# Kernel tuning notes

Measured on AMD Instinct MI355X. Metric: run time of the kernel, lower is better.

Reference implementation:

```python
import jax, jax.numpy as jnp
import numpy as np

# Module config (matches init_kwargs)
B, C, T, H, W = 8, 64, 50, 64, 64
KH = KW = 2          # kernel_size
SH = SW = 2          # stride
DH = DW = 1          # dilation
HO = (H - (KH - 1) * DH - 1) // SH + 1  # 32
WO = (W - (KW - 1) * DW - 1) // SW + 1  # 32


def setup_inputs() -> dict:
    key = jax.random.key(0)
    x = jax.random.uniform(key, (B, C, T, H, W), dtype=jnp.float32)
    return {"x": x}


def reference(x):
    b, c, t, h, w = x.shape
    # temporal cumsum then sum over time (mode '2D')
    x_sum = jnp.cumsum(x, axis=2).sum(axis=2)  # (B, C, H, W)

    # max_pool2d with flat (row-major, per-channel H*W) indices, torch semantics
    hh = (jnp.arange(HO) * SH)[:, None] + jnp.arange(KH) * DH  # (HO, KH)
    ww = (jnp.arange(WO) * SW)[:, None] + jnp.arange(KW) * DW  # (WO, KW)
    win = x_sum[:, :, hh, :][..., ww]                     # (B, C, HO, KH, WO, KW)
    win = win.transpose(0, 1, 2, 4, 3, 5).reshape(b, c, HO, WO, KH * KW)
    # flat H*W index of each window element, row-major within window
    flat = (hh[:, None, :, None] * w + ww[None, :, None, :]).reshape(HO, WO, KH * KW)
    amax = jnp.argmax(win, axis=-1)                       # first max, like torch
    flat_b = jnp.broadcast_to(flat, (b, c, HO, WO, KH * KW))
    indices_2d = jnp.take_along_axis(flat_b, amax[..., None], axis=-1)[..., 0]  # (B,C,HO,WO)

    # gather the winning spatial location at every timestep
    x_flat = x.reshape(b, c, t, h * w)
    idx = jnp.broadcast_to(indices_2d.reshape(b, c, 1, HO * WO), (b, c, t, HO * WO))
    spk_rec = jnp.take_along_axis(x_flat, idx, axis=3).reshape(b, c, t, HO, WO)

    loss = 0.0 * spk_rec.mean()
    return spk_rec, loss
```

## Files before the change

kernel.cpp:

```cpp
#include <hip/hip_runtime.h>

#define BB 8
#define CC 64
#define TT 50
#define HH 64
#define WW 64
#define HO 32
#define WO 32
#define PLANE (HH * WW)
#define BC_STRIDE (TT * PLANE)
#define OUT_T_STRIDE (HO * WO)
#define OUT_BC_STRIDE (TT * OUT_T_STRIDE)
#define N_OUT_MAIN (BB * CC * OUT_BC_STRIDE)

__global__ __launch_bounds__(256, 3)
void spike_pool_kernel(const float* __restrict__ x, float* __restrict__ out) {
    const int blk = blockIdx.x;
    const int bc  = blk >> 3;
    const int R   = blk & 7;
    const int tid = threadIdx.x;

    const float2* __restrict__ base =
        (const float2*)(x + (size_t)bc * BC_STRIDE + R * 8 * WW);

    float2 pix[TT];
    float c0 = 0.f, c1 = 0.f, s0 = 0.f, s1 = 0.f;
#pragma unroll
    for (int t = 0; t < TT; ++t) {
        float2 v = base[(size_t)t * (PLANE / 2) + tid];
        pix[t] = v;
        c0 += v.x; s0 += c0;
        c1 += v.y; s1 += c1;
    }

    const float os0 = __shfl_xor(s0, 32);
    const float os1 = __shfl_xor(s1, 32);
    const bool top = ((tid >> 5) & 1) == 0;
    const float v0 = top ? s0  : os0;
    const float v1 = top ? s1  : os1;
    const float v2 = top ? os0 : s0;
    const float v3 = top ? os1 : s1;
    int win = 0; float bv = v0;
    if (v1 > bv) { bv = v1; win = 1; }
    if (v2 > bv) { bv = v2; win = 2; }
    if (v3 > bv) { bv = v3; win = 3; }

    const int  col       = win & 1;
    const bool needCross = top ? (win >= 2) : (win < 2);

    float* __restrict__ obase = out + (size_t)bc * OUT_BC_STRIDE
                              + (size_t)(R * 4 + (tid >> 6)) * WO + (tid & 31);

#pragma unroll
    for (int t = 0; t < TT; t += 2) {
        const float m0 = col ? pix[t].y     : pix[t].x;
        const float m1 = col ? pix[t + 1].y : pix[t + 1].x;
        const float x0 = __shfl_xor(m0, 32);
        const float x1 = __shfl_xor(m1, 32);
        if (top) obase[(size_t)t       * OUT_T_STRIDE] = needCross ? x0 : m0;
        else     obase[(size_t)(t + 1) * OUT_T_STRIDE] = needCross ? x1 : m1;
    }

    if (blk == 0 && tid == 0) out[N_OUT_MAIN] = 0.0f;
}

extern "C" void kernel_launch(void* const* d_in, const int* in_sizes, int n_in,
                              void* d_out, int out_size, void* d_ws, size_t ws_size,
                              hipStream_t stream) {
    const float* x = (const float*)d_in[0];
    float* out = (float*)d_out;
    dim3 grid(BB * CC * (HH / 8));
    dim3 block(256);
    spike_pool_kernel<<<grid, block, 0, stream>>>(x, out);
}
```

Baseline: 646.7 us.

## Widen per-thread work to float4 loads, float2 nontemporal stores

```diff
diff --git a/kernel.cpp b/kernel.cpp
--- a/kernel.cpp
+++ b/kernel.cpp
@@ -13,52 +13,84 @@
 #define OUT_BC_STRIDE (TT * OUT_T_STRIDE)
 #define N_OUT_MAIN (BB * CC * OUT_BC_STRIDE)
 
-__global__ __launch_bounds__(256, 3)
+typedef float f2_t __attribute__((ext_vector_type(2)));
+
+__global__ __launch_bounds__(256, 2)
 void spike_pool_kernel(const float* __restrict__ x, float* __restrict__ out) {
     const int blk = blockIdx.x;
-    const int bc  = blk >> 3;
-    const int R   = blk & 7;
+    const int bc  = blk >> 2;
+    const int R   = blk & 3;
     const int tid = threadIdx.x;
 
-    const float2* __restrict__ base =
-        (const float2*)(x + (size_t)bc * BC_STRIDE + R * 8 * WW);
+    const float4* __restrict__ base =
+        (const float4*)(x + (size_t)bc * BC_STRIDE + R * 16 * WW);
 
-    float2 pix[TT];
-    float c0 = 0.f, c1 = 0.f, s0 = 0.f, s1 = 0.f;
+    float4 pix[TT];
+    float cx = 0.f, cy = 0.f, cz = 0.f, cw = 0.f;
+    float sx = 0.f, sy = 0.f, sz = 0.f, sw = 0.f;
 #pragma unroll
     for (int t = 0; t < TT; ++t) {
-        float2 v = base[(size_t)t * (PLANE / 2) + tid];
+        float4 v = base[(size_t)t * (PLANE / 4) + tid];
         pix[t] = v;
-        c0 += v.x; s0 += c0;
-        c1 += v.y; s1 += c1;
+        cx += v.x; sx += cx;
+        cy += v.y; sy += cy;
+        cz += v.z; sz += cz;
+        cw += v.w; sw += cw;
     }
 
-    const float os0 = __shfl_xor(s0, 32);
-    const float os1 = __shfl_xor(s1, 32);
-    const bool top = ((tid >> 5) & 1) == 0;
-    const float v0 = top ? s0  : os0;
-    const float v1 = top ? s1  : os1;
-    const float v2 = top ? os0 : s0;
-    const float v3 = top ? os1 : s1;
-    int win = 0; float bv = v0;
-    if (v1 > bv) { bv = v1; win = 1; }
-    if (v2 > bv) { bv = v2; win = 2; }
-    if (v3 > bv) { bv = v3; win = 3; }
+    const float ox_ = __shfl_xor(sx, 16);
+    const float oy_ = __shfl_xor(sy, 16);
+    const float oz_ = __shfl_xor(sz, 16);
+    const float ow_ = __shfl_xor(sw, 16);
+    const bool top = ((tid >> 4) & 1) == 0;
 
-    const int  col       = win & 1;
-    const bool needCross = top ? (win >= 2) : (win < 2);
+    const float w0a = top ? sx  : ox_;
+    const float w0b = top ? sy  : oy_;
+    const float w0c = top ? ox_ : sx;
+    const float w0d = top ? oy_ : sy;
+    int win0 = 0; float bv0 = w0a;
+    if (w0b > bv0) { bv0 = w0b; win0 = 1; }
+    if (w0c > bv0) { bv0 = w0c; win0 = 2; }
+    if (w0d > bv0) { bv0 = w0d; win0 = 3; }
+
+    const float w1a = top ? sz  : oz_;
+    const float w1b = top ? sw  : ow_;
+    const float w1c = top ? oz_ : sz;
+    const float w1d = top ? ow_ : sw;
+    int win1 = 0; float bv1 = w1a;
+    if (w1b > bv1) { bv1 = w1b; win1 = 1; }
+    if (w1c > bv1) { bv1 = w1c; win1 = 2; }
+    if (w1d > bv1) { bv1 = w1d; win1 = 3; }
+
+    const int  col0 = win0 & 1, col1 = win1 & 1;
+    const bool cross0 = top ? (win0 >= 2) : (win0 < 2);
+    const bool cross1 = top ? (win1 >= 2) : (win1 < 2);
 
     float* __restrict__ obase = out + (size_t)bc * OUT_BC_STRIDE
-                              + (size_t)(R * 4 + (tid >> 6)) * WO + (tid & 31);
+                              + (size_t)(R * 8 + ((tid >> 4) >> 1)) * WO
+                              + 2 * (tid & 15);
 
 #pragma unroll
     for (int t = 0; t < TT; t += 2) {
-        const float m0 = col ? pix[t].y     : pix[t].x;
-        const float m1 = col ? pix[t + 1].y : pix[t + 1].x;
-        const float x0 = __shfl_xor(m0, 32);
-        const float x1 = __shfl_xor(m1, 32);
-        if (top) obase[(size_t)t       * OUT_T_STRIDE] = needCross ? x0 : m0;
-        else     obase[(size_t)(t + 1) * OUT_T_STRIDE] = needCross ? x1 : m1;
+        const float a0 = col0 ? pix[t].y     : pix[t].x;
+        const float a1 = col1 ? pix[t].w     : pix[t].z;
+        const float b0 = col0 ? pix[t + 1].y : pix[t + 1].x;
+        const float b1 = col1 ? pix[t + 1].w : pix[t + 1].z;
+        const float xa0 = __shfl_xor(a0, 16);
+        const float xa1 = __shfl_xor(a1, 16);
+        const float xb0 = __shfl_xor(b0, 16);
+        const float xb1 = __shfl_xor(b1, 16);
+        f2_t o; size_t off;
+        if (top) {
+            o.x = cross0 ? xa0 : a0;
+            o.y = cross1 ? xa1 : a1;
+            off = (size_t)t * OUT_T_STRIDE;
+        } else {
+            o.x = cross0 ? xb0 : b0;
+            o.y = cross1 ? xb1 : b1;
+            off = (size_t)(t + 1) * OUT_T_STRIDE;
+        }
+        __builtin_nontemporal_store(o, (f2_t*)(obase + off));
     }
 
     if (blk == 0 && tid == 0) out[N_OUT_MAIN] = 0.0f;
@@ -69,7 +101,7 @@
                               hipStream_t stream) {
     const float* x = (const float*)d_in[0];
     float* out = (float*)d_out;
-    dim3 grid(BB * CC * (HH / 8));
+    dim3 grid(BB * CC * (HH / 16));
     dim3 block(256);
     spike_pool_kernel<<<grid, block, 0, stream>>>(x, out);
 }
```

Measured after the change: 665.1 us. +2.9%, slower.
